# Optimization experiments

Hardware: AMD Instinct MI355X
Metric: run time of the kernel (lower is better)

Reference implementation:

```python
import jax, jax.numpy as jnp
import numpy as np


def setup_inputs() -> dict:
    key = jax.random.key(0)
    ks = jax.random.split(key, 8)
    n_src, n_dst, n_edges = 100000, 50000, 600000
    d_in, d_out = 128, 128
    n_reuse, n_cache = 5000, 8000
    full_dst_len = n_dst + n_reuse

    feat_src = jax.random.normal(ks[0], (n_src, d_in), jnp.float32)
    src = jax.random.randint(ks[1], (n_edges,), 0, n_src)
    dst = jax.random.randint(ks[2], (n_edges,), 0, n_dst)
    # xavier-ish init for the two bias-free Linear layers (stored as [out, in] like torch)
    W_self = jax.random.normal(ks[3], (d_out, d_in), jnp.float32) / np.sqrt(d_in).astype(np.float32)
    W_neigh = jax.random.normal(ks[4], (d_out, d_in), jnp.float32) / np.sqrt(d_in).astype(np.float32)
    # reuse_indices must be unique positions within [0, full_dst_len)
    reuse_indices = jnp.sort(jax.random.permutation(ks[5], full_dst_len)[:n_reuse])
    reuse_embedding = jax.random.normal(ks[6], (n_reuse, d_out), jnp.float32)
    cache_indices = jax.random.randint(ks[7], (n_cache,), 0, full_dst_len)
    return dict(feat_src=feat_src, W_self=W_self, W_neigh=W_neigh,
                reuse_embedding=reuse_embedding, src=src, dst=dst,
                reuse_indices=reuse_indices, cache_indices=cache_indices,
                n_dst=n_dst)


def reference(feat_src, W_self, W_neigh, reuse_embedding, src, dst,
              reuse_indices, cache_indices, n_dst):
    # --- GraphSAGE 'mean' aggregation on a block graph ---
    feat_dst = feat_src[:n_dst]                         # [n_dst, D_in]
    msgs = feat_src[src]                                # [E, D_in] copy_src gather
    ssum = jax.ops.segment_sum(msgs, dst, num_segments=n_dst)          # [n_dst, D_in]
    deg = jax.ops.segment_sum(jnp.ones_like(msgs[:, 0]), dst, num_segments=n_dst)
    h_neigh = jnp.where(deg[:, None] > 0, ssum / jnp.maximum(deg, 1.0)[:, None], 0.0)
    rst = feat_dst @ W_self.T + h_neigh @ W_neigh.T     # fc_self + fc_neigh

    # --- cache-reuse scatter merge (flag == 0 path) ---
    n_reuse = reuse_indices.shape[0]
    full_dst_len = n_dst + n_reuse
    keep = jnp.ones((full_dst_len,), dtype=bool).at[reuse_indices].set(False)
    unprune_indices = jnp.nonzero(keep, size=n_dst)[0]  # np.delete equivalent
    full = jnp.zeros((full_dst_len, rst.shape[1]), rst.dtype)
    full = full.at[unprune_indices].set(rst).at[reuse_indices].set(reuse_embedding)
    cache_embedding = jax.lax.stop_gradient(full[cache_indices])  # .detach()
    return full, cache_embedding
```

## Files before the change

kernel.cpp:

```cpp
#include <hip/hip_runtime.h>

#define N_SRC   100000
#define N_DST   50000
#define D       128
#define MAXDEG  64

#define TOTAL_BLOCKS 2048
#define EDGE_BLOCKS  512

typedef __attribute__((ext_vector_type(8))) short bf16x8;
typedef __attribute__((ext_vector_type(4))) float f32x4;

__device__ __forceinline__ unsigned short f2bf(float f) {
    unsigned u = __float_as_uint(f);
    u += 0x7FFFu + ((u >> 16) & 1u);
    return (unsigned short)(u >> 16);
}
__device__ __forceinline__ float bf2f(unsigned short u) {
    return __uint_as_float((unsigned)u << 16);
}

__global__ __launch_bounds__(256)
void prep_build_kernel(const int* __restrict__ src,
                       const int* __restrict__ dst,
                       int* __restrict__ ell,
                       int* __restrict__ cnt,
                       int n_edges,
                       const int* __restrict__ reuse_idx,
                       int* __restrict__ rowpos, int n_reuse,
                       const float* __restrict__ Wself,
                       const float* __restrict__ Wneigh,
                       unsigned short* __restrict__ wbf,
                       const float* __restrict__ feat,
                       unsigned int* __restrict__ featbf_u32) {
    if (blockIdx.x < EDGE_BLOCKS) {
        int eid = blockIdx.x * 256 + threadIdx.x;
        const int estride = EDGE_BLOCKS * 256;
        for (int e = eid; e < n_edges; e += estride) {
            int d = dst[e];
            int pos = atomicAdd(&cnt[d], 1);
            if (pos < MAXDEG)
                ell[(size_t)d * MAXDEG + pos] = src[e];
        }
    } else {
        int stid = (blockIdx.x - EDGE_BLOCKS) * 256 + threadIdx.x;
        const int sstride = (TOTAL_BLOCKS - EDGE_BLOCKS) * 256;

        if (stid < N_DST) {
            int lo = 0, hi = n_reuse;
            while (lo < hi) {
                int mid = (lo + hi) >> 1;
                if (reuse_idx[mid] - mid > stid) hi = mid; else lo = mid + 1;
            }
            rowpos[stid] = stid + lo;
        }

        if (stid < 128 * 256) {
            int n = stid >> 8;
            int k = stid & 255;
            float v = (k < 128) ? Wself[n * 128 + k] : Wneigh[n * 128 + (k - 128)];
            wbf[stid] = f2bf(v);
        }

        const int n4 = N_SRC * (D / 4);
        for (int i = stid; i < n4; i += sstride) {
            float4 v = *(const float4*)(feat + (size_t)i * 4);
            uint2 o;
            o.x = (unsigned)f2bf(v.x) | ((unsigned)f2bf(v.y) << 16);
            o.y = (unsigned)f2bf(v.z) | ((unsigned)f2bf(v.w) << 16);
            *(uint2*)(featbf_u32 + (size_t)i * 2) = o;
        }
    }
}

__global__ __launch_bounds__(256)
void gather_bf16_kernel(const unsigned short* __restrict__ featbf,
                        const int* __restrict__ ell,
                        const int* __restrict__ cnt,
                        uint4* __restrict__ hneigh_u4) {
    int gid  = blockIdx.x * blockDim.x + threadIdx.x;
    int row  = gid >> 4;
    int lane = gid & 15;
    if (row >= N_DST) return;

    int deg = cnt[row];
    int n = min(deg, MAXDEG);
    float inv = 1.0f / fmaxf((float)deg, 1.0f);
    const int* rell = ell + (size_t)row * MAXDEG;

    float acc[8];
#pragma unroll
    for (int k = 0; k < 8; ++k) acc[k] = 0.f;

    union U { uint4 v; unsigned short us[8]; };
    int j = 0;
    for (; j + 4 <= n; j += 4) {
        int s0 = rell[j + 0];
        int s1 = rell[j + 1];
        int s2 = rell[j + 2];
        int s3 = rell[j + 3];
        U a, b, c, d;
        a.v = *(const uint4*)(featbf + (size_t)s0 * D + lane * 8);
        b.v = *(const uint4*)(featbf + (size_t)s1 * D + lane * 8);
        c.v = *(const uint4*)(featbf + (size_t)s2 * D + lane * 8);
        d.v = *(const uint4*)(featbf + (size_t)s3 * D + lane * 8);
#pragma unroll
        for (int k = 0; k < 8; ++k)
            acc[k] += (bf2f(a.us[k]) + bf2f(b.us[k])) + (bf2f(c.us[k]) + bf2f(d.us[k]));
    }
    for (; j < n; ++j) {
        int s = rell[j];
        U a;
        a.v = *(const uint4*)(featbf + (size_t)s * D + lane * 8);
#pragma unroll
        for (int k = 0; k < 8; ++k) acc[k] += bf2f(a.us[k]);
    }
    uint4 o;
    o.x = (unsigned)f2bf(acc[0] * inv) | ((unsigned)f2bf(acc[1] * inv) << 16);
    o.y = (unsigned)f2bf(acc[2] * inv) | ((unsigned)f2bf(acc[3] * inv) << 16);
    o.z = (unsigned)f2bf(acc[4] * inv) | ((unsigned)f2bf(acc[5] * inv) << 16);
    o.w = (unsigned)f2bf(acc[6] * inv) | ((unsigned)f2bf(acc[7] * inv) << 16);
    hneigh_u4[(size_t)row * 16 + lane] = o;
}

__global__ __launch_bounds__(256, 2)
void gemm_kernel(const unsigned short* __restrict__ featbf,
                 const unsigned short* __restrict__ hneigh,
                 const unsigned short* __restrict__ wbf,
                 const int* __restrict__ rowpos,
                 float* __restrict__ full) {
    __shared__ unsigned short Wl[128 * 256];

    int tid = threadIdx.x;
    {
        int n = tid >> 1;
        int ckbase = (tid & 1) * 16;
        const uint4* s = (const uint4*)(wbf + n * 256);
        uint4* d = (uint4*)(Wl + n * 256);
#pragma unroll
        for (int i = 0; i < 16; ++i) {
            int ck = ckbase + i;
            d[ck ^ (n & 7)] = s[ck];
        }
    }
    __syncthreads();

    int wv   = tid >> 6;
    int lane = tid & 63;
    int l15  = lane & 15;
    int q    = lane >> 4;
    int rowbase = blockIdx.x * 128 + wv * 32;

    f32x4 acc[2][8];
#pragma unroll
    for (int rt = 0; rt < 2; ++rt)
#pragma unroll
        for (int ct = 0; ct < 8; ++ct) acc[rt][ct] = (f32x4){0.f, 0.f, 0.f, 0.f};

    int r0c = min(rowbase + l15,      N_DST - 1);
    int r1c = min(rowbase + 16 + l15, N_DST - 1);

#pragma unroll
    for (int s = 0; s < 8; ++s) {
        const unsigned short* A = (s < 4) ? featbf : hneigh;
        int k0 = (s & 3) * 32 + q * 8;
        bf16x8 a0 = *(const bf16x8*)(A + (size_t)r0c * D + k0);
        bf16x8 a1 = *(const bf16x8*)(A + (size_t)r1c * D + k0);
#pragma unroll
        for (int ct = 0; ct < 8; ++ct) {
            int n = ct * 16 + l15;
            int ck = s * 4 + q;
            bf16x8 b = *(const bf16x8*)(Wl + n * 256 + ((ck ^ (n & 7)) << 3));
            acc[0][ct] = __builtin_amdgcn_mfma_f32_16x16x32_bf16(a0, b, acc[0][ct], 0, 0, 0);
            acc[1][ct] = __builtin_amdgcn_mfma_f32_16x16x32_bf16(a1, b, acc[1][ct], 0, 0, 0);
        }
    }

#pragma unroll
    for (int rt = 0; rt < 2; ++rt) {
#pragma unroll
        for (int reg = 0; reg < 4; ++reg) {
            int gm = rowbase + rt * 16 + q * 4 + reg;
            if (gm < N_DST) {
                int jj = rowpos[gm];
                float* outr = full + (size_t)jj * D + l15;
#pragma unroll
                for (int ct = 0; ct < 8; ++ct)
                    outr[ct * 16] = acc[rt][ct][reg];
            }
        }
    }
}

__global__ __launch_bounds__(256, 2)
void gemm_f32a_kernel(const float* __restrict__ feat,
                      const unsigned short* __restrict__ hneigh,
                      const unsigned short* __restrict__ wbf,
                      const int* __restrict__ rowpos,
                      float* __restrict__ full) {
    __shared__ unsigned short Wl[128 * 256];

    int tid = threadIdx.x;
    {
        int n = tid >> 1;
        int ckbase = (tid & 1) * 16;
        const uint4* s = (const uint4*)(wbf + n * 256);
        uint4* d = (uint4*)(Wl + n * 256);
#pragma unroll
        for (int i = 0; i < 16; ++i) {
            int ck = ckbase + i;
            d[ck ^ (n & 7)] = s[ck];
        }
    }
    __syncthreads();

    int wv   = tid >> 6;
    int lane = tid & 63;
    int l15  = lane & 15;
    int q    = lane >> 4;
    int rowbase = blockIdx.x * 128 + wv * 32;

    f32x4 acc[2][8];
#pragma unroll
    for (int rt = 0; rt < 2; ++rt)
#pragma unroll
        for (int ct = 0; ct < 8; ++ct) acc[rt][ct] = (f32x4){0.f, 0.f, 0.f, 0.f};

    int r0c = min(rowbase + l15,      N_DST - 1);
    int r1c = min(rowbase + 16 + l15, N_DST - 1);

#pragma unroll 1
    for (int s = 0; s < 4; ++s) {
        int k0 = s * 32 + q * 8;
        float4 a0lo = *(const float4*)(feat + (size_t)r0c * D + k0);
        float4 a0hi = *(const float4*)(feat + (size_t)r0c * D + k0 + 4);
        float4 a1lo = *(const float4*)(feat + (size_t)r1c * D + k0);
        float4 a1hi = *(const float4*)(feat + (size_t)r1c * D + k0 + 4);
        union { bf16x8 v; unsigned short u[8]; } a0, a1;
        a0.u[0] = f2bf(a0lo.x); a0.u[1] = f2bf(a0lo.y);
        a0.u[2] = f2bf(a0lo.z); a0.u[3] = f2bf(a0lo.w);
        a0.u[4] = f2bf(a0hi.x); a0.u[5] = f2bf(a0hi.y);
        a0.u[6] = f2bf(a0hi.z); a0.u[7] = f2bf(a0hi.w);
        a1.u[0] = f2bf(a1lo.x); a1.u[1] = f2bf(a1lo.y);
        a1.u[2] = f2bf(a1lo.z); a1.u[3] = f2bf(a1lo.w);
        a1.u[4] = f2bf(a1hi.x); a1.u[5] = f2bf(a1hi.y);
        a1.u[6] = f2bf(a1hi.z); a1.u[7] = f2bf(a1hi.w);
#pragma unroll
        for (int ct = 0; ct < 8; ++ct) {
            int n = ct * 16 + l15;
            int ck = s * 4 + q;
            bf16x8 b = *(const bf16x8*)(Wl + n * 256 + ((ck ^ (n & 7)) << 3));
            acc[0][ct] = __builtin_amdgcn_mfma_f32_16x16x32_bf16(a0.v, b, acc[0][ct], 0, 0, 0);
            acc[1][ct] = __builtin_amdgcn_mfma_f32_16x16x32_bf16(a1.v, b, acc[1][ct], 0, 0, 0);
        }
    }
#pragma unroll 1
    for (int s = 0; s < 4; ++s) {
        int k0 = s * 32 + q * 8;
        bf16x8 a0 = *(const bf16x8*)(hneigh + (size_t)r0c * D + k0);
        bf16x8 a1 = *(const bf16x8*)(hneigh + (size_t)r1c * D + k0);
#pragma unroll
        for (int ct = 0; ct < 8; ++ct) {
            int n = ct * 16 + l15;
            int ck = 16 + s * 4 + q;
            bf16x8 b = *(const bf16x8*)(Wl + n * 256 + ((ck ^ (n & 7)) << 3));
            acc[0][ct] = __builtin_amdgcn_mfma_f32_16x16x32_bf16(a0, b, acc[0][ct], 0, 0, 0);
            acc[1][ct] = __builtin_amdgcn_mfma_f32_16x16x32_bf16(a1, b, acc[1][ct], 0, 0, 0);
        }
    }

#pragma unroll
    for (int rt = 0; rt < 2; ++rt) {
#pragma unroll
        for (int reg = 0; reg < 4; ++reg) {
            int gm = rowbase + rt * 16 + q * 4 + reg;
            if (gm < N_DST) {
                int jj = rowpos[gm];
                float* outr = full + (size_t)jj * D + l15;
#pragma unroll
                for (int ct = 0; ct < 8; ++ct)
                    outr[ct * 16] = acc[rt][ct][reg];
            }
        }
    }
}

__global__ __launch_bounds__(256)
void epilogue_kernel(const float* __restrict__ emb,
                     const int* __restrict__ ridx, int n_reuse,
                     float* __restrict__ full,
                     const int* __restrict__ cidx,
                     float* __restrict__ cache_out, int n_cache) {
    int idx = blockIdx.x * blockDim.x + threadIdx.x;
    int row = idx >> 5;
    int c4 = (idx & 31) * 4;
    if (row < n_reuse) {
        *(float4*)&full[(size_t)ridx[row] * D + c4] =
            *(const float4*)&emb[(size_t)row * D + c4];
    } else if (row < n_reuse + n_cache) {
        int r = row - n_reuse;
        int v = cidx[r];
        int lo = 0, hi = n_reuse;
        while (lo < hi) {
            int mid = (lo + hi) >> 1;
            if (ridx[mid] < v) lo = mid + 1; else hi = mid;
        }
        const float* srcp = (lo < n_reuse && ridx[lo] == v)
            ? emb + (size_t)lo * D
            : full + (size_t)v * D;
        *(float4*)&cache_out[(size_t)r * D + c4] = *(const float4*)&srcp[c4];
    }
}

extern "C" void kernel_launch(void* const* d_in, const int* in_sizes, int n_in,
                              void* d_out, int out_size, void* d_ws, size_t ws_size,
                              hipStream_t stream) {
    const float* feat_src  = (const float*)d_in[0];
    const float* W_self    = (const float*)d_in[1];
    const float* W_neigh   = (const float*)d_in[2];
    const float* reuse_emb = (const float*)d_in[3];
    const int*   src       = (const int*)d_in[4];
    const int*   dst       = (const int*)d_in[5];
    const int*   reuse_idx = (const int*)d_in[6];
    const int*   cache_idx = (const int*)d_in[7];

    int n_edges = in_sizes[4];
    int n_reuse = in_sizes[6];
    int n_cache = in_sizes[7];
    int full_len = N_DST + n_reuse;

    float* full = (float*)d_out;
    float* cache_out = full + (size_t)full_len * D;

    size_t hneigh_b = (size_t)N_DST * D * sizeof(unsigned short);
    size_t featbf_b = (size_t)N_SRC * D * sizeof(unsigned short);
    size_t ell_b    = (size_t)N_DST * MAXDEG * sizeof(int);
    size_t small_b  = 2 * (size_t)N_DST * 4 + 128 * 256 * 2;
    size_t need_fast = hneigh_b + featbf_b + small_b;

    int ep_rows = n_reuse + n_cache;

    if (ws_size >= need_fast) {
        unsigned short* hneigh = (unsigned short*)d_ws;
        unsigned short* featbf = (unsigned short*)((char*)d_ws + hneigh_b);
        int*   cnt    = (int*)((char*)featbf + featbf_b);
        int*   rowpos = cnt + N_DST;
        unsigned short* wbf = (unsigned short*)(rowpos + N_DST);
        int* ell = (int*)full;

        hipMemsetAsync(cnt, 0, (size_t)N_DST * sizeof(int), stream);

        prep_build_kernel<<<TOTAL_BLOCKS, 256, 0, stream>>>(
            src, dst, ell, cnt, n_edges,
            reuse_idx, rowpos, n_reuse, W_self, W_neigh, wbf,
            feat_src, (unsigned int*)featbf);

        gather_bf16_kernel<<<(N_DST * 16 + 255) / 256, 256, 0, stream>>>(
            featbf, ell, cnt, (uint4*)hneigh);

        gemm_kernel<<<(N_DST + 127) / 128, 256, 0, stream>>>(
            featbf, hneigh, wbf, rowpos, full);

        epilogue_kernel<<<(ep_rows * 32 + 255) / 256, 256, 0, stream>>>(
            reuse_emb, reuse_idx, n_reuse, full, cache_idx, cache_out, n_cache);
    } else {
        unsigned short* hneigh = (unsigned short*)d_ws;
        int*   ell    = (int*)((char*)d_ws + hneigh_b);
        int*   cnt    = (int*)((char*)ell + ell_b);
        int*   rowpos = cnt + N_DST;
        unsigned short* wbf = (unsigned short*)(rowpos + N_DST);
        unsigned short* featbf = (unsigned short*)full;

        hipMemsetAsync(cnt, 0, (size_t)N_DST * sizeof(int), stream);

        prep_build_kernel<<<TOTAL_BLOCKS, 256, 0, stream>>>(
            src, dst, ell, cnt, n_edges,
            reuse_idx, rowpos, n_reuse, W_self, W_neigh, wbf,
            feat_src, (unsigned int*)featbf);

        gather_bf16_kernel<<<(N_DST * 16 + 255) / 256, 256, 0, stream>>>(
            featbf, ell, cnt, (uint4*)hneigh);

        gemm_f32a_kernel<<<(N_DST + 127) / 128, 256, 0, stream>>>(
            feat_src, hneigh, wbf, rowpos, full);

        epilogue_kernel<<<(ep_rows * 32 + 255) / 256, 256, 0, stream>>>(
            reuse_emb, reuse_idx, n_reuse, full, cache_idx, cache_out, n_cache);
    }
}
```

Measured before the change: 186.0 us.

## Split per-destination edge counters into eight sub-lists to reduce atomic contention

Edge bucketing now spreads each destination's atomics across eight counter copies (chosen by edge index), with 16 slots each, so colliding atomicAdds on one counter are reduced. The gather kernel sums the eight counts for the degree and walks each sub-list. Edge-building blocks grow from 512 to 1024, and the fallback path for small workspaces is removed. The risk is that a sub-list can overflow at 16 entries, silently dropping neighbours where the old cap was 64, and the counter memset is eight times larger.

Result: slower. 206.1 us (+10.8%).

```diff
diff --git a/kernel.cpp b/kernel.cpp
--- a/kernel.cpp
+++ b/kernel.cpp
@@ -3,10 +3,11 @@
 #define N_SRC   100000
 #define N_DST   50000
 #define D       128
-#define MAXDEG  64
+#define NCOPY   8
+#define CSLOTS  16
 
 #define TOTAL_BLOCKS 2048
-#define EDGE_BLOCKS  512
+#define EDGE_BLOCKS  1024
 
 typedef __attribute__((ext_vector_type(8))) short bf16x8;
 typedef __attribute__((ext_vector_type(4))) float f32x4;
@@ -24,7 +25,7 @@
 void prep_build_kernel(const int* __restrict__ src,
                        const int* __restrict__ dst,
                        int* __restrict__ ell,
-                       int* __restrict__ cnt,
+                       int* __restrict__ cnt8,
                        int n_edges,
                        const int* __restrict__ reuse_idx,
                        int* __restrict__ rowpos, int n_reuse,
@@ -38,9 +39,11 @@
         const int estride = EDGE_BLOCKS * 256;
         for (int e = eid; e < n_edges; e += estride) {
             int d = dst[e];
-            int pos = atomicAdd(&cnt[d], 1);
-            if (pos < MAXDEG)
-                ell[(size_t)d * MAXDEG + pos] = src[e];
+            int s = src[e];
+            int c = e & (NCOPY - 1);
+            int pos = atomicAdd(&cnt8[d * NCOPY + c], 1);
+            if (pos < CSLOTS)
+                ell[((size_t)d * NCOPY + c) * CSLOTS + pos] = s;
         }
     } else {
         int stid = (blockIdx.x - EDGE_BLOCKS) * 256 + threadIdx.x;
@@ -76,44 +79,51 @@
 __global__ __launch_bounds__(256)
 void gather_bf16_kernel(const unsigned short* __restrict__ featbf,
                         const int* __restrict__ ell,
-                        const int* __restrict__ cnt,
+                        const int* __restrict__ cnt8,
                         uint4* __restrict__ hneigh_u4) {
     int gid  = blockIdx.x * blockDim.x + threadIdx.x;
     int row  = gid >> 4;
     int lane = gid & 15;
     if (row >= N_DST) return;
 
-    int deg = cnt[row];
-    int n = min(deg, MAXDEG);
+    const int* cc = cnt8 + (size_t)row * NCOPY;
+    int4 ca = *(const int4*)cc;
+    int4 cb = *(const int4*)(cc + 4);
+    int cnts[8] = {ca.x, ca.y, ca.z, ca.w, cb.x, cb.y, cb.z, cb.w};
+    int deg = 0;
+#pragma unroll
+    for (int c = 0; c < 8; ++c) deg += cnts[c];
     float inv = 1.0f / fmaxf((float)deg, 1.0f);
-    const int* rell = ell + (size_t)row * MAXDEG;
+
+    const int* rell = ell + (size_t)row * (NCOPY * CSLOTS);
 
     float acc[8];
 #pragma unroll
     for (int k = 0; k < 8; ++k) acc[k] = 0.f;
 
     union U { uint4 v; unsigned short us[8]; };
-    int j = 0;
-    for (; j + 4 <= n; j += 4) {
-        int s0 = rell[j + 0];
-        int s1 = rell[j + 1];
-        int s2 = rell[j + 2];
-        int s3 = rell[j + 3];
-        U a, b, c, d;
-        a.v = *(const uint4*)(featbf + (size_t)s0 * D + lane * 8);
-        b.v = *(const uint4*)(featbf + (size_t)s1 * D + lane * 8);
-        c.v = *(const uint4*)(featbf + (size_t)s2 * D + lane * 8);
-        d.v = *(const uint4*)(featbf + (size_t)s3 * D + lane * 8);
-#pragma unroll
-        for (int k = 0; k < 8; ++k)
-            acc[k] += (bf2f(a.us[k]) + bf2f(b.us[k])) + (bf2f(c.us[k]) + bf2f(d.us[k]));
-    }
-    for (; j < n; ++j) {
-        int s = rell[j];
-        U a;
-        a.v = *(const uint4*)(featbf + (size_t)s * D + lane * 8);
-#pragma unroll
-        for (int k = 0; k < 8; ++k) acc[k] += bf2f(a.us[k]);
+#pragma unroll 1
+    for (int c = 0; c < NCOPY; ++c) {
+        int nc = min(cnts[c], CSLOTS);
+        const int* lst = rell + c * CSLOTS;
+        int j = 0;
+        for (; j + 2 <= nc; j += 2) {
+            int s0 = lst[j];
+            int s1 = lst[j + 1];
+            U a, b;
+            a.v = *(const uint4*)(featbf + (size_t)s0 * D + lane * 8);
+            b.v = *(const uint4*)(featbf + (size_t)s1 * D + lane * 8);
+#pragma unroll
+            for (int k = 0; k < 8; ++k)
+                acc[k] += bf2f(a.us[k]) + bf2f(b.us[k]);
+        }
+        if (j < nc) {
+            int s = lst[j];
+            U a;
+            a.v = *(const uint4*)(featbf + (size_t)s * D + lane * 8);
+#pragma unroll
+            for (int k = 0; k < 8; ++k) acc[k] += bf2f(a.us[k]);
+        }
     }
     uint4 o;
     o.x = (unsigned)f2bf(acc[0] * inv) | ((unsigned)f2bf(acc[1] * inv) << 16);
@@ -170,99 +180,6 @@
         for (int ct = 0; ct < 8; ++ct) {
             int n = ct * 16 + l15;
             int ck = s * 4 + q;
-            bf16x8 b = *(const bf16x8*)(Wl + n * 256 + ((ck ^ (n & 7)) << 3));
-            acc[0][ct] = __builtin_amdgcn_mfma_f32_16x16x32_bf16(a0, b, acc[0][ct], 0, 0, 0);
-            acc[1][ct] = __builtin_amdgcn_mfma_f32_16x16x32_bf16(a1, b, acc[1][ct], 0, 0, 0);
-        }
-    }
-
-#pragma unroll
-    for (int rt = 0; rt < 2; ++rt) {
-#pragma unroll
-        for (int reg = 0; reg < 4; ++reg) {
-            int gm = rowbase + rt * 16 + q * 4 + reg;
-            if (gm < N_DST) {
-                int jj = rowpos[gm];
-                float* outr = full + (size_t)jj * D + l15;
-#pragma unroll
-                for (int ct = 0; ct < 8; ++ct)
-                    outr[ct * 16] = acc[rt][ct][reg];
-            }
-        }
-    }
-}
-
-__global__ __launch_bounds__(256, 2)
-void gemm_f32a_kernel(const float* __restrict__ feat,
-                      const unsigned short* __restrict__ hneigh,
-                      const unsigned short* __restrict__ wbf,
-                      const int* __restrict__ rowpos,
-                      float* __restrict__ full) {
-    __shared__ unsigned short Wl[128 * 256];
-
-    int tid = threadIdx.x;
-    {
-        int n = tid >> 1;
-        int ckbase = (tid & 1) * 16;
-        const uint4* s = (const uint4*)(wbf + n * 256);
-        uint4* d = (uint4*)(Wl + n * 256);
-#pragma unroll
-        for (int i = 0; i < 16; ++i) {
-            int ck = ckbase + i;
-            d[ck ^ (n & 7)] = s[ck];
-        }
-    }
-    __syncthreads();
-
-    int wv   = tid >> 6;
-    int lane = tid & 63;
-    int l15  = lane & 15;
-    int q    = lane >> 4;
-    int rowbase = blockIdx.x * 128 + wv * 32;
-
-    f32x4 acc[2][8];
-#pragma unroll
-    for (int rt = 0; rt < 2; ++rt)
-#pragma unroll
-        for (int ct = 0; ct < 8; ++ct) acc[rt][ct] = (f32x4){0.f, 0.f, 0.f, 0.f};
-
-    int r0c = min(rowbase + l15,      N_DST - 1);
-    int r1c = min(rowbase + 16 + l15, N_DST - 1);
-
-#pragma unroll 1
-    for (int s = 0; s < 4; ++s) {
-        int k0 = s * 32 + q * 8;
-        float4 a0lo = *(const float4*)(feat + (size_t)r0c * D + k0);
-        float4 a0hi = *(const float4*)(feat + (size_t)r0c * D + k0 + 4);
-        float4 a1lo = *(const float4*)(feat + (size_t)r1c * D + k0);
-        float4 a1hi = *(const float4*)(feat + (size_t)r1c * D + k0 + 4);
-        union { bf16x8 v; unsigned short u[8]; } a0, a1;
-        a0.u[0] = f2bf(a0lo.x); a0.u[1] = f2bf(a0lo.y);
-        a0.u[2] = f2bf(a0lo.z); a0.u[3] = f2bf(a0lo.w);
-        a0.u[4] = f2bf(a0hi.x); a0.u[5] = f2bf(a0hi.y);
-        a0.u[6] = f2bf(a0hi.z); a0.u[7] = f2bf(a0hi.w);
-        a1.u[0] = f2bf(a1lo.x); a1.u[1] = f2bf(a1lo.y);
-        a1.u[2] = f2bf(a1lo.z); a1.u[3] = f2bf(a1lo.w);
-        a1.u[4] = f2bf(a1hi.x); a1.u[5] = f2bf(a1hi.y);
-        a1.u[6] = f2bf(a1hi.z); a1.u[7] = f2bf(a1hi.w);
-#pragma unroll
-        for (int ct = 0; ct < 8; ++ct) {
-            int n = ct * 16 + l15;
-            int ck = s * 4 + q;
-            bf16x8 b = *(const bf16x8*)(Wl + n * 256 + ((ck ^ (n & 7)) << 3));
-            acc[0][ct] = __builtin_amdgcn_mfma_f32_16x16x32_bf16(a0.v, b, acc[0][ct], 0, 0, 0);
-            acc[1][ct] = __builtin_amdgcn_mfma_f32_16x16x32_bf16(a1.v, b, acc[1][ct], 0, 0, 0);
-        }
-    }
-#pragma unroll 1
-    for (int s = 0; s < 4; ++s) {
-        int k0 = s * 32 + q * 8;
-        bf16x8 a0 = *(const bf16x8*)(hneigh + (size_t)r0c * D + k0);
-        bf16x8 a1 = *(const bf16x8*)(hneigh + (size_t)r1c * D + k0);
-#pragma unroll
-        for (int ct = 0; ct < 8; ++ct) {
-            int n = ct * 16 + l15;
-            int ck = 16 + s * 4 + q;
             bf16x8 b = *(const bf16x8*)(Wl + n * 256 + ((ck ^ (n & 7)) << 3));
             acc[0][ct] = __builtin_amdgcn_mfma_f32_16x16x32_bf16(a0, b, acc[0][ct], 0, 0, 0);
             acc[1][ct] = __builtin_amdgcn_mfma_f32_16x16x32_bf16(a1, b, acc[1][ct], 0, 0, 0);
@@ -334,57 +251,29 @@
 
     size_t hneigh_b = (size_t)N_DST * D * sizeof(unsigned short);
     size_t featbf_b = (size_t)N_SRC * D * sizeof(unsigned short);
-    size_t ell_b    = (size_t)N_DST * MAXDEG * sizeof(int);
-    size_t small_b  = 2 * (size_t)N_DST * 4 + 128 * 256 * 2;
-    size_t need_fast = hneigh_b + featbf_b + small_b;
-
-    int ep_rows = n_reuse + n_cache;
-
-    if (ws_size >= need_fast) {
-        unsigned short* hneigh = (unsigned short*)d_ws;
-        unsigned short* featbf = (unsigned short*)((char*)d_ws + hneigh_b);
-        int*   cnt    = (int*)((char*)featbf + featbf_b);
-        int*   rowpos = cnt + N_DST;
-        unsigned short* wbf = (unsigned short*)(rowpos + N_DST);
-        int* ell = (int*)full;
-
-        hipMemsetAsync(cnt, 0, (size_t)N_DST * sizeof(int), stream);
-
-        prep_build_kernel<<<TOTAL_BLOCKS, 256, 0, stream>>>(
-            src, dst, ell, cnt, n_edges,
-            reuse_idx, rowpos, n_reuse, W_self, W_neigh, wbf,
-            feat_src, (unsigned int*)featbf);
-
-        gather_bf16_kernel<<<(N_DST * 16 + 255) / 256, 256, 0, stream>>>(
-            featbf, ell, cnt, (uint4*)hneigh);
-
-        gemm_kernel<<<(N_DST + 127) / 128, 256, 0, stream>>>(
-            featbf, hneigh, wbf, rowpos, full);
-
-        epilogue_kernel<<<(ep_rows * 32 + 255) / 256, 256, 0, stream>>>(
-            reuse_emb, reuse_idx, n_reuse, full, cache_idx, cache_out, n_cache);
-    } else {
-        unsigned short* hneigh = (unsigned short*)d_ws;
-        int*   ell    = (int*)((char*)d_ws + hneigh_b);
-        int*   cnt    = (int*)((char*)ell + ell_b);
-        int*   rowpos = cnt + N_DST;
-        unsigned short* wbf = (unsigned short*)(rowpos + N_DST);
-        unsigned short* featbf = (unsigned short*)full;
-
-        hipMemsetAsync(cnt, 0, (size_t)N_DST * sizeof(int), stream);
-
-        prep_build_kernel<<<TOTAL_BLOCKS, 256, 0, stream>>>(
-            src, dst, ell, cnt, n_edges,
-            reuse_idx, rowpos, n_reuse, W_self, W_neigh, wbf,
-            feat_src, (unsigned int*)featbf);
-
-        gather_bf16_kernel<<<(N_DST * 16 + 255) / 256, 256, 0, stream>>>(
-            featbf, ell, cnt, (uint4*)hneigh);
-
-        gemm_f32a_kernel<<<(N_DST + 127) / 128, 256, 0, stream>>>(
-            feat_src, hneigh, wbf, rowpos, full);
-
-        epilogue_kernel<<<(ep_rows * 32 + 255) / 256, 256, 0, stream>>>(
-            reuse_emb, reuse_idx, n_reuse, full, cache_idx, cache_out, n_cache);
-    }
-}
+    size_t cnt8_b   = (size_t)N_DST * NCOPY * sizeof(int);
+
+    unsigned short* hneigh = (unsigned short*)d_ws;
+    unsigned short* featbf = (unsigned short*)((char*)d_ws + hneigh_b);
+    int*   cnt8   = (int*)((char*)featbf + featbf_b);
+    int*   rowpos = (int*)((char*)cnt8 + cnt8_b);
+    unsigned short* wbf = (unsigned short*)(rowpos + N_DST);
+
+    int* ell = (int*)full;
+
+    hipMemsetAsync(cnt8, 0, cnt8_b, stream);
+
+    prep_build_kernel<<<TOTAL_BLOCKS, 256, 0, stream>>>(
+        src, dst, ell, cnt8, n_edges,
+        reuse_idx, rowpos, n_reuse, W_self, W_neigh, wbf,
+        feat_src, (unsigned int*)featbf);
+
+    gather_bf16_kernel<<<(N_DST * 16 + 255) / 256, 256, 0, stream>>>(
+        featbf, ell, cnt8, (uint4*)hneigh);
+
+    gemm_kernel<<<(N_DST + 127) / 128, 256, 0, stream>>>(
+        featbf, hneigh, wbf, rowpos, full);
+
+    epilogue_kernel<<<((n_reuse + n_cache) * 32 + 255) / 256, 256, 0, stream>>>(
+        reuse_emb, reuse_idx, n_reuse, full, cache_idx, cache_out, n_cache);
+}
```
